# Optimization experiments

Hardware: AMD Instinct MI355X
Metric: run time of the kernel (lower is better)

## Reference

```python
import jax, jax.numpy as jnp
import numpy as np

B, T, C, Hh, Ww = 4, 24, 128, 48, 48
N_HEAD, D_K, D_MODEL = 16, 4, 128
D_PE = D_MODEL // N_HEAD  # 8
T_PERIOD = 1000.0


def group_norm(x, gamma, beta, groups, eps=1e-5):
    # x: (N, C) or (N, C, L); normalize over each group's channels (+ trailing dims)
    shp = x.shape
    xg = x.reshape(shp[0], groups, -1)
    mu = xg.mean(-1, keepdims=True)
    var = xg.var(-1, keepdims=True)
    xn = ((xg - mu) * jax.lax.rsqrt(var + eps)).reshape(shp)
    bshape = (1, shp[1]) + (1,) * (len(shp) - 2)
    return xn * gamma.reshape(bshape) + beta.reshape(bshape)


def _lin(k, fi, fo, std):
    kw, _ = jax.random.split(k)
    return jax.random.normal(kw, (fo, fi), jnp.float32) * std, jnp.zeros((fo,), jnp.float32)


def setup_inputs():
    key = jax.random.key(0)
    ks = jax.random.split(key, 8)
    std_k = float(np.sqrt(2.0 / D_K))
    p = {}
    p['x'] = jax.random.normal(ks[0], (B, T, C, Hh, Ww), jnp.float32)
    p['batch_positions'] = jnp.sort(jax.random.randint(ks[1], (B, T), 0, 365), axis=1).astype(jnp.int32)
    # inconv: 128 -> 256 -> 128, each Linear + GroupNorm(4) + ReLU
    p['w_in0'], p['b_in0'] = _lin(ks[2], C, 256, float(np.sqrt(2.0 / C)))
    p['g_in0'], p['be_in0'] = jnp.ones((256,), jnp.float32), jnp.zeros((256,), jnp.float32)
    p['w_in1'], p['b_in1'] = _lin(ks[3], 256, D_MODEL, float(np.sqrt(2.0 / 256)))
    p['g_in1'], p['be_in1'] = jnp.ones((D_MODEL,), jnp.float32), jnp.zeros((D_MODEL,), jnp.float32)
    # in_norm GroupNorm(16, 128)
    p['g_innorm'], p['b_innorm'] = jnp.ones((D_MODEL,), jnp.float32), jnp.zeros((D_MODEL,), jnp.float32)
    # attention: fixed query + key projection
    p['Q'] = jax.random.normal(ks[4], (N_HEAD, D_K), jnp.float32) * std_k
    p['w_k'], p['b_k'] = _lin(ks[5], D_MODEL, N_HEAD * D_K, std_k)
    # output MLP: 128 -> 256 -> 128
    p['w_m0'], p['b_m0'] = _lin(ks[6], D_MODEL, 256, float(np.sqrt(2.0 / D_MODEL)))
    p['g_m0'], p['be_m0'] = jnp.ones((256,), jnp.float32), jnp.zeros((256,), jnp.float32)
    p['w_m1'], p['b_m1'] = _lin(ks[7], 256, 128, float(np.sqrt(2.0 / 256)))
    p['g_m1'], p['be_m1'] = jnp.ones((128,), jnp.float32), jnp.zeros((128,), jnp.float32)
    # out_norm GroupNorm(16, 128)
    p['g_out'], p['b_out'] = jnp.ones((128,), jnp.float32), jnp.zeros((128,), jnp.float32)
    return p


def ltae_forward(x, pos_f, w_in0, b_in0, g_in0, be_in0, w_in1, b_in1, g_in1, be_in1,
                 g_innorm, b_innorm, Q, w_k, b_k,
                 w_m0, b_m0, g_m0, be_m0, w_m1, b_m1, g_m1, be_m1, g_out, b_out):
    Bsz, Ts, Cc, Hp, Wp = x.shape
    N = Bsz * Hp * Wp
    # (B,T,C,H,W) -> (B,H,W,T,C) -> (N, T, C): one sequence per pixel
    out = x.transpose(0, 3, 4, 1, 2).reshape(N, Ts, Cc)
    # inconv MLP on flattened tokens
    h = out.reshape(N * Ts, Cc)
    h = jax.nn.relu(group_norm(h @ w_in0.T + b_in0, g_in0, be_in0, 4))
    h = jax.nn.relu(group_norm(h @ w_in1.T + b_in1, g_in1, be_in1, 4))
    out = h.reshape(N, Ts, D_MODEL)
    # in_norm: GroupNorm(n_head) over (C, T)
    out = group_norm(out.transpose(0, 2, 1), g_innorm, b_innorm, N_HEAD).transpose(0, 2, 1)
    # positional encoding (d_model//n_head sinusoid, tiled n_head times)
    idx = jnp.arange(D_PE)
    denom = T_PERIOD ** (2.0 * (idx // 2).astype(jnp.float32) / D_PE)
    tab = pos_f[:, :, None] / denom  # (B, T, D_PE)
    tab = jnp.where(idx % 2 == 0, jnp.sin(tab), jnp.cos(tab))
    pe = jnp.tile(tab, (1, 1, N_HEAD))  # (B, T, D_MODEL)
    out = (out.reshape(Bsz, Hp * Wp, Ts, D_MODEL) + pe[:, None]).reshape(N, Ts, D_MODEL)
    # fixed-query multi-head attention
    k = (out @ w_k.T + b_k).reshape(N, Ts, N_HEAD, D_K)
    scores = jnp.einsum('hk,nthk->nht', Q, k) / jnp.sqrt(jnp.float32(D_K))
    a = jax.nn.softmax(scores, axis=-1)  # (N, H, T)
    v = out.reshape(N, Ts, N_HEAD, D_MODEL // N_HEAD)
    o = jnp.einsum('nht,nthv->nhv', a, v).reshape(N, D_MODEL)
    # output MLP + out_norm
    m = jax.nn.relu(group_norm(o @ w_m0.T + b_m0, g_m0, be_m0, 4))
    m = jax.nn.relu(group_norm(m @ w_m1.T + b_m1, g_m1, be_m1, 4))
    y = group_norm(m, g_out, b_out, N_HEAD)
    return y.reshape(Bsz, Hp, Wp, -1).transpose(0, 3, 1, 2)  # (B, C_out, H, W)


def reference(x, batch_positions, w_in0, b_in0, g_in0, be_in0, w_in1, b_in1, g_in1, be_in1,
              g_innorm, b_innorm, Q, w_k, b_k,
              w_m0, b_m0, g_m0, be_m0, w_m1, b_m1, g_m1, be_m1, g_out, b_out):
    pos_f = batch_positions.astype(jnp.float32)
    return ltae_forward(x, pos_f, w_in0, b_in0, g_in0, be_in0, w_in1, b_in1, g_in1, be_in1,
                        g_innorm, b_innorm, Q, w_k, b_k,
                        w_m0, b_m0, g_m0, be_m0, w_m1, b_m1, g_m1, be_m1, g_out, b_out)
```

## Files before the change

kernel.cpp:

```cpp
#include <hip/hip_runtime.h>
#include <math.h>

typedef _Float16 f16x8 __attribute__((ext_vector_type(8)));
typedef float f32x4 __attribute__((ext_vector_type(4)));
typedef unsigned short ushort_t;

constexpr int HWp = 2304;
constexpr float EPS = 1e-5f;

constexpr size_t M0P_OFF = 273472;
constexpr size_t M1P_OFF = 404544;
constexpr size_t OWS_OFF = 535616;

__device__ __forceinline__ int sidx(int row, int c) {
    return ((row << 8) + ((c << 1) ^ ((row & 7) << 4))) >> 1;
}
__device__ __forceinline__ int sidx2(int row, int c) {
    return ((row << 7) + ((c << 1) ^ ((row & 7) << 4))) >> 1;
}

__global__ void ltae_prep(const float* __restrict__ w_in0, const float* __restrict__ w_in1,
                          const float* __restrict__ Qm, const float* __restrict__ w_k,
                          const float* __restrict__ b_k, const int* __restrict__ bpos,
                          const float* __restrict__ w_m0, const float* __restrict__ w_m1,
                          _Float16* __restrict__ w1h, _Float16* __restrict__ w1l,
                          _Float16* __restrict__ w2h, _Float16* __restrict__ w2l,
                          _Float16* __restrict__ qkBh, _Float16* __restrict__ qkBl,
                          float* __restrict__ qb2G, float* __restrict__ peG,
                          float* __restrict__ w_m0P, float* __restrict__ w_m1P) {
    int i = blockIdx.x * 256 + threadIdx.x;
    if (i < 32768) {
        float v = w_in0[i];
        _Float16 h = (_Float16)v;
        w1h[i] = h; w1l[i] = (_Float16)(v - (float)h);
    } else if (i < 65536) {
        int j = i - 32768;
        float v = w_in1[j];
        _Float16 h = (_Float16)v;
        w2h[j] = h; w2l[j] = (_Float16)(v - (float)h);
    } else if (i < 67584) {
        int j = i - 65536; int h = j >> 7, k = j & 127;
        float s = 0.f;
        #pragma unroll
        for (int dk = 0; dk < 4; dk++) s = fmaf(Qm[h * 4 + dk], w_k[(h * 4 + dk) * 128 + k], s);
        s *= 0.5f;
        _Float16 hi = (_Float16)s;
        int ks = k >> 5, lg = (k >> 3) & 3, jj = k & 7;
        int pos = ((ks * 4 + lg) * 16 + h) * 8 + jj;
        qkBh[pos] = hi; qkBl[pos] = (_Float16)(s - (float)hi);
    } else if (i < 67600) {
        int h = i - 67584;
        float s = 0.f;
        #pragma unroll
        for (int dk = 0; dk < 4; dk++) s = fmaf(Qm[h * 4 + dk], b_k[h * 4 + dk], s);
        qb2G[h] = 0.5f * s;
    } else if (i < 68368) {
        int j = i - 67600;
        int bb = j / 192, r = j - bb * 192;
        int t = r >> 3, d = r & 7;
        const float dens[4] = {1.0f, 5.623413251903491f, 31.622776601683793f, 177.82794100389228f};
        float ang = (float)bpos[bb * 24 + t] / dens[d >> 1];
        peG[j] = (d & 1) ? cosf(ang) : sinf(ang);
    } else if (i < 101136) {
        int j = i - 68368;
        int c2 = j >> 9, rem = j & 511, o = rem >> 1, jj = rem & 1;
        w_m0P[j] = w_m0[o * 128 + c2 * 2 + jj];
    } else if (i < 133904) {
        int j = i - 101136;
        int c2 = j >> 8, rem = j & 255, o = rem >> 1, jj = rem & 1;
        w_m1P[j] = w_m1[o * 256 + c2 * 2 + jj];
    }
}

__global__ __launch_bounds__(256, 3) void ltae_main(
    const float* __restrict__ x,
    const float* __restrict__ b_in0, const float* __restrict__ g_in0, const float* __restrict__ be_in0,
    const float* __restrict__ b_in1, const float* __restrict__ g_in1, const float* __restrict__ be_in1,
    const float* __restrict__ g_innorm, const float* __restrict__ b_innorm,
    const _Float16* __restrict__ w1h, const _Float16* __restrict__ w1l,
    const _Float16* __restrict__ w2h, const _Float16* __restrict__ w2l,
    const _Float16* __restrict__ qkBh, const _Float16* __restrict__ qkBl,
    const float* __restrict__ qb2G, const float* __restrict__ peG,
    float* __restrict__ o_ws)
{
    __shared__ __align__(16) ushort_t Ah[48 * 128], Al[48 * 128];
    __shared__ __align__(16) ushort_t Hh[48 * 64], Hl[48 * 64];
    __shared__ float peS[24][8];
    __shared__ float2 partS[192];

    float* scP = (float*)Hh;

    const int tid = threadIdx.x;
    const int bid = blockIdx.x;
    const int sb  = (bid & 7) * 576 + (bid >> 3);
    const int b   = sb / 1152;
    const int pixbase = (sb - b * 1152) * 2;
    const int w  = tid >> 6;
    const int l  = tid & 63;
    const int lr = l & 15;
    const int lg = l >> 4;

    if (tid < 192) peS[tid >> 3][tid & 7] = peG[b * 192 + tid];
    for (int i = tid; i < 24 * 128; i += 256) {
        int t = i >> 7, c = i & 127;
        const float* gp = x + ((size_t)((b * 24 + t) * 128 + c)) * HWp + pixbase;
        float2 v = *(const float2*)gp;
        _Float16 h0 = (_Float16)v.x;
        _Float16 h1 = (_Float16)v.y;
        int i0 = sidx(t, c), i1 = sidx(24 + t, c);
        Ah[i0] = __builtin_bit_cast(ushort_t, h0);
        Al[i0] = __builtin_bit_cast(ushort_t, (_Float16)(v.x - (float)h0));
        Ah[i1] = __builtin_bit_cast(ushort_t, h1);
        Al[i1] = __builtin_bit_cast(ushort_t, (_Float16)(v.y - (float)h1));
    }
    __syncthreads();

    f32x4 acc2[3][2];
    #pragma unroll
    for (int m = 0; m < 3; m++)
        #pragma unroll
        for (int nt = 0; nt < 2; nt++) acc2[m][nt] = f32x4{0.f, 0.f, 0.f, 0.f};
    const int n2 = w * 32 + lr;

    #pragma unroll 1
    for (int q = 0; q < 4; q++) {
        const int n1 = q * 64 + w * 16 + lr;
        f16x8 bh[4], bl[4];
        #pragma unroll
        for (int ks = 0; ks < 4; ks++) {
            bh[ks] = *(const f16x8*)(w1h + n1 * 128 + ks * 32 + lg * 8);
            bl[ks] = *(const f16x8*)(w1l + n1 * 128 + ks * 32 + lg * 8);
        }
        const float gg = g_in0[n1], bb = be_in0[n1], bi = b_in0[n1];

        f32x4 acc1[3];
        #pragma unroll
        for (int m = 0; m < 3; m++) acc1[m] = f32x4{0.f, 0.f, 0.f, 0.f};
        #pragma unroll
        for (int m = 0; m < 3; m++) {
            #pragma unroll
            for (int ks = 0; ks < 4; ks++) {
                f16x8 ah = *(const f16x8*)&Ah[sidx(m * 16 + lr, ks * 32 + lg * 8)];
                f16x8 al = *(const f16x8*)&Al[sidx(m * 16 + lr, ks * 32 + lg * 8)];
                acc1[m] = __builtin_amdgcn_mfma_f32_16x16x32_f16(ah, bl[ks], acc1[m], 0, 0, 0);
                acc1[m] = __builtin_amdgcn_mfma_f32_16x16x32_f16(al, bh[ks], acc1[m], 0, 0, 0);
                acc1[m] = __builtin_amdgcn_mfma_f32_16x16x32_f16(ah, bh[ks], acc1[m], 0, 0, 0);
            }
        }
        float ps[3][4], ps2[3][4];
        #pragma unroll
        for (int m = 0; m < 3; m++) {
            #pragma unroll
            for (int r = 0; r < 4; r++) {
                float v = acc1[m][r] + bi;
                float s = v, s2 = v * v;
                #pragma unroll
                for (int mk = 1; mk <= 8; mk <<= 1) { s += __shfl_xor(s, mk); s2 += __shfl_xor(s2, mk); }
                ps[m][r] = s; ps2[m][r] = s2;
            }
        }
        if (lr == 0) {
            #pragma unroll
            for (int m = 0; m < 3; m++)
                #pragma unroll
                for (int r = 0; r < 4; r++)
                    partS[w * 48 + m * 16 + lg * 4 + r] = make_float2(ps[m][r], ps2[m][r]);
        }
        __syncthreads();
        #pragma unroll
        for (int m = 0; m < 3; m++) {
            #pragma unroll
            for (int r = 0; r < 4; r++) {
                int idx = m * 16 + lg * 4 + r;
                float st = 0.f, s2t = 0.f;
                #pragma unroll
                for (int j = 0; j < 4; j++) {
                    float2 qv = partS[j * 48 + idx];
                    st += qv.x; s2t += qv.y;
                }
                float mu = st * (1.f / 64.f);
                float rs = rsqrtf(s2t * (1.f / 64.f) - mu * mu + EPS);
                float v = acc1[m][r] + bi;
                float hv = fmaxf(fmaf((v - mu) * rs, gg, bb), 0.f);
                _Float16 h16 = (_Float16)hv;
                int ii = sidx2(idx, w * 16 + lr);
                Hh[ii] = __builtin_bit_cast(ushort_t, h16);
                Hl[ii] = __builtin_bit_cast(ushort_t, (_Float16)(hv - (float)h16));
            }
        }
        __syncthreads();

        f16x8 b2h[2][2], b2l[2][2];
        #pragma unroll
        for (int nt = 0; nt < 2; nt++) {
            int n = n2 + nt * 16;
            #pragma unroll
            for (int ks = 0; ks < 2; ks++) {
                b2h[nt][ks] = *(const f16x8*)(w2h + n * 256 + q * 64 + ks * 32 + lg * 8);
                b2l[nt][ks] = *(const f16x8*)(w2l + n * 256 + q * 64 + ks * 32 + lg * 8);
            }
        }
        #pragma unroll
        for (int m = 0; m < 3; m++) {
            #pragma unroll
            for (int ks = 0; ks < 2; ks++) {
                f16x8 ah = *(const f16x8*)&Hh[sidx2(m * 16 + lr, ks * 32 + lg * 8)];
                f16x8 al = *(const f16x8*)&Hl[sidx2(m * 16 + lr, ks * 32 + lg * 8)];
                #pragma unroll
                for (int nt = 0; nt < 2; nt++) {
                    acc2[m][nt] = __builtin_amdgcn_mfma_f32_16x16x32_f16(ah, b2l[nt][ks], acc2[m][nt], 0, 0, 0);
                    acc2[m][nt] = __builtin_amdgcn_mfma_f32_16x16x32_f16(al, b2h[nt][ks], acc2[m][nt], 0, 0, 0);
                    acc2[m][nt] = __builtin_amdgcn_mfma_f32_16x16x32_f16(ah, b2h[nt][ks], acc2[m][nt], 0, 0, 0);
                }
            }
        }
        __syncthreads();
    }

    {
        const int cA = w * 32 + lr;
        const int cB = cA + 16;
        float b2v[2]  = {b_in1[cA], b_in1[cB]};
        float g2v[2]  = {g_in1[cA], g_in1[cB]};
        float be2v[2] = {be_in1[cA], be_in1[cB]};
        float giV[2]  = {g_innorm[cA], g_innorm[cB]};
        float biV[2]  = {b_innorm[cA], b_innorm[cB]};

        float hv[3][4][2];
        #pragma unroll
        for (int m = 0; m < 3; m++) {
            #pragma unroll
            for (int r = 0; r < 4; r++) {
                float v0 = acc2[m][0][r] + b2v[0], v1 = acc2[m][1][r] + b2v[1];
                float s = v0 + v1, s2 = v0 * v0 + v1 * v1;
                #pragma unroll
                for (int mk = 1; mk <= 8; mk <<= 1) { s += __shfl_xor(s, mk); s2 += __shfl_xor(s2, mk); }
                float mu = s * (1.f / 32.f);
                float rs = rsqrtf(s2 * (1.f / 32.f) - mu * mu + EPS);
                hv[m][r][0] = fmaxf(fmaf((v0 - mu) * rs, g2v[0], be2v[0]), 0.f);
                hv[m][r][1] = fmaxf(fmaf((v1 - mu) * rs, g2v[1], be2v[1]), 0.f);
            }
        }
        float s0[2] = {0.f, 0.f}, s02[2] = {0.f, 0.f};
        float s1[2] = {0.f, 0.f}, s12[2] = {0.f, 0.f};
        #pragma unroll
        for (int m = 0; m < 3; m++) {
            #pragma unroll
            for (int r = 0; r < 4; r++) {
                int row = m * 16 + lg * 4 + r;
                #pragma unroll
                for (int nt = 0; nt < 2; nt++) {
                    float v = hv[m][r][nt];
                    if (row >= 24) { s1[nt] += v; s12[nt] += v * v; }
                    else           { s0[nt] += v; s02[nt] += v * v; }
                }
            }
        }
        #pragma unroll
        for (int nt = 0; nt < 2; nt++) {
            #pragma unroll
            for (int mk = 0; mk < 5; mk++) {
                int msk = (mk < 3) ? (1 << mk) : (2 << mk);
                s0[nt] += __shfl_xor(s0[nt], msk);  s02[nt] += __shfl_xor(s02[nt], msk);
                s1[nt] += __shfl_xor(s1[nt], msk);  s12[nt] += __shfl_xor(s12[nt], msk);
            }
        }
        float mu0[2], rs0[2], mu1[2], rs1[2];
        #pragma unroll
        for (int nt = 0; nt < 2; nt++) {
            mu0[nt] = s0[nt] * (1.f / 192.f);
            rs0[nt] = rsqrtf(s02[nt] * (1.f / 192.f) - mu0[nt] * mu0[nt] + EPS);
            mu1[nt] = s1[nt] * (1.f / 192.f);
            rs1[nt] = rsqrtf(s12[nt] * (1.f / 192.f) - mu1[nt] * mu1[nt] + EPS);
        }
        #pragma unroll
        for (int m = 0; m < 3; m++) {
            #pragma unroll
            for (int r = 0; r < 4; r++) {
                int row = m * 16 + lg * 4 + r;
                int p1 = row >= 24;
                int t = row - (p1 ? 24 : 0);
                float pe = peS[t][lr & 7];
                #pragma unroll
                for (int nt = 0; nt < 2; nt++) {
                    float mu = p1 ? mu1[nt] : mu0[nt];
                    float rs = p1 ? rs1[nt] : rs0[nt];
                    float v = fmaf((hv[m][r][nt] - mu) * rs, giV[nt], biV[nt]) + pe;
                    _Float16 h16 = (_Float16)v;
                    int ii = sidx(row, w * 32 + nt * 16 + lr);
                    Ah[ii] = __builtin_bit_cast(ushort_t, h16);
                    Al[ii] = __builtin_bit_cast(ushort_t, (_Float16)(v - (float)h16));
                }
            }
        }
    }
    __syncthreads();

    if (w < 3) {
        const int m = w;
        f16x8 qh[4], ql[4];
        #pragma unroll
        for (int ks = 0; ks < 4; ks++) {
            qh[ks] = *(const f16x8*)(qkBh + ((ks * 4 + lg) * 16 + lr) * 8);
            ql[ks] = *(const f16x8*)(qkBl + ((ks * 4 + lg) * 16 + lr) * 8);
        }
        f32x4 sacc = f32x4{0.f, 0.f, 0.f, 0.f};
        #pragma unroll
        for (int ks = 0; ks < 4; ks++) {
            f16x8 ah = *(const f16x8*)&Ah[sidx(m * 16 + lr, ks * 32 + lg * 8)];
            f16x8 al = *(const f16x8*)&Al[sidx(m * 16 + lr, ks * 32 + lg * 8)];
            sacc = __builtin_amdgcn_mfma_f32_16x16x32_f16(ah, ql[ks], sacc, 0, 0, 0);
            sacc = __builtin_amdgcn_mfma_f32_16x16x32_f16(al, qh[ks], sacc, 0, 0, 0);
            sacc = __builtin_amdgcn_mfma_f32_16x16x32_f16(ah, qh[ks], sacc, 0, 0, 0);
        }
        float qb = qb2G[lr];
        #pragma unroll
        for (int r = 0; r < 4; r++) {
            int row = m * 16 + lg * 4 + r;
            int p = row >= 24 ? 1 : 0;
            int t = row - p * 24;
            scP[(p * 16 + lr) * 24 + t] = sacc[r] + qb;
        }
    }
    __syncthreads();

    {
        const int p = w >> 1;
        int h = (w & 1) * 8 + (l >> 3), j = l & 7;
        float* sp = scP + (p * 16 + h) * 24;
        float mx = -1e30f;
        #pragma unroll
        for (int k = 0; k < 3; k++) mx = fmaxf(mx, sp[j + 8 * k]);
        mx = fmaxf(mx, __shfl_xor(mx, 1));
        mx = fmaxf(mx, __shfl_xor(mx, 2));
        mx = fmaxf(mx, __shfl_xor(mx, 4));
        float ev[3], sum = 0.f;
        #pragma unroll
        for (int k = 0; k < 3; k++) { ev[k] = __expf(sp[j + 8 * k] - mx); sum += ev[k]; }
        sum += __shfl_xor(sum, 1);
        sum += __shfl_xor(sum, 2);
        sum += __shfl_xor(sum, 4);
        float inv = 1.f / sum;
        #pragma unroll
        for (int k = 0; k < 3; k++) sp[j + 8 * k] = ev[k] * inv;
    }

    {
        const int p = w >> 1;
        int ch = (w & 1) * 64 + l;
        int h = ch >> 3;
        const float* sp = scP + (p * 16 + h) * 24;
        float s = 0.f;
        #pragma unroll
        for (int t = 0; t < 24; t++) {
            int ii = sidx(p * 24 + t, ch);
            float v = (float)__builtin_bit_cast(_Float16, Ah[ii]) +
                      (float)__builtin_bit_cast(_Float16, Al[ii]);
            s = fmaf(sp[t], v, s);
        }
        o_ws[((size_t)(b * 2304 + pixbase + p)) * 128 + ch] = s;
    }
}

__global__ __launch_bounds__(256) void ltae_mlp(
    const float* __restrict__ o_ws,
    const float* __restrict__ w_m0P, const float* __restrict__ b_m0,
    const float* __restrict__ g_m0, const float* __restrict__ be_m0,
    const float* __restrict__ w_m1P, const float* __restrict__ b_m1,
    const float* __restrict__ g_m1, const float* __restrict__ be_m1,
    const float* __restrict__ g_out, const float* __restrict__ b_out,
    float* __restrict__ out)
{
    __shared__ float ovP[8 * 128];
    __shared__ float mmP[8 * 256];
    float* ysP = ovP;

    const int tid = threadIdx.x;
    const int bid = blockIdx.x;
    const int b = bid / 288;
    const int pix8 = (bid - b * 288) * 8;

    #pragma unroll
    for (int k = 0; k < 4; k++) {
        int i = tid + (k << 8);
        ovP[i] = o_ws[((size_t)(b * 2304 + pix8)) * 128 + i];
    }
    __syncthreads();

    {
        const int o = tid;
        float acc[8];
        #pragma unroll
        for (int pp = 0; pp < 8; pp++) acc[pp] = 0.f;
        for (int c2 = 0; c2 < 64; c2++) {
            float2 w2 = *(const float2*)(w_m0P + c2 * 512 + o * 2);
            #pragma unroll
            for (int pp = 0; pp < 8; pp++) {
                float2 x2 = *(const float2*)(ovP + pp * 128 + c2 * 2);
                acc[pp] = fmaf(w2.x, x2.x, acc[pp]);
                acc[pp] = fmaf(w2.y, x2.y, acc[pp]);
            }
        }
        float bi = b_m0[o], gg = g_m0[o], bb = be_m0[o];
        #pragma unroll
        for (int pp = 0; pp < 8; pp++) {
            float v = acc[pp] + bi;
            float s = v, s2 = v * v;
            #pragma unroll
            for (int mk = 1; mk <= 32; mk <<= 1) { s += __shfl_xor(s, mk); s2 += __shfl_xor(s2, mk); }
            float mu = s * (1.f / 64.f);
            float rs = rsqrtf(s2 * (1.f / 64.f) - mu * mu + EPS);
            mmP[pp * 256 + o] = fmaxf(fmaf((v - mu) * rs, gg, bb), 0.f);
        }
    }
    __syncthreads();

    {
        const int o = tid & 127, hw = tid >> 7;
        float acc[4];
        #pragma unroll
        for (int q = 0; q < 4; q++) acc[q] = 0.f;
        for (int c2 = 0; c2 < 128; c2++) {
            float2 w2 = *(const float2*)(w_m1P + c2 * 256 + o * 2);
            #pragma unroll
            for (int q = 0; q < 4; q++) {
                float2 x2 = *(const float2*)(mmP + (hw * 4 + q) * 256 + c2 * 2);
                acc[q] = fmaf(w2.x, x2.x, acc[q]);
                acc[q] = fmaf(w2.y, x2.y, acc[q]);
            }
        }
        float bm1 = b_m1[o], gm1 = g_m1[o], bem1 = be_m1[o];
        float go = g_out[o], bo = b_out[o];
        #pragma unroll
        for (int q = 0; q < 4; q++) {
            const int pp = hw * 4 + q;
            float v = acc[q] + bm1;
            float s = v, s2 = v * v;
            #pragma unroll
            for (int mk = 1; mk <= 16; mk <<= 1) { s += __shfl_xor(s, mk); s2 += __shfl_xor(s2, mk); }
            float mu = s * (1.f / 32.f);
            float rs = rsqrtf(s2 * (1.f / 32.f) - mu * mu + EPS);
            float v2 = fmaxf(fmaf((v - mu) * rs, gm1, bem1), 0.f);
            float t1 = v2, t2 = v2 * v2;
            #pragma unroll
            for (int mk = 1; mk <= 4; mk <<= 1) { t1 += __shfl_xor(t1, mk); t2 += __shfl_xor(t2, mk); }
            float mu2 = t1 * (1.f / 8.f);
            float rs2 = rsqrtf(t2 * (1.f / 8.f) - mu2 * mu2 + EPS);
            ysP[pp * 128 + o] = fmaf((v2 - mu2) * rs2, go, bo);
        }
    }
    __syncthreads();

    {
        const int o = tid & 127, q4 = (tid >> 7) * 4;
        float4 y4;
        y4.x = ysP[(q4 + 0) * 128 + o];
        y4.y = ysP[(q4 + 1) * 128 + o];
        y4.z = ysP[(q4 + 2) * 128 + o];
        y4.w = ysP[(q4 + 3) * 128 + o];
        *(float4*)(out + ((size_t)(b * 128 + o)) * HWp + pix8 + q4) = y4;
    }
}

extern "C" void kernel_launch(void* const* d_in, const int* in_sizes, int n_in,
                              void* d_out, int out_size, void* d_ws, size_t ws_size,
                              hipStream_t stream) {
    const float* x        = (const float*)d_in[0];
    const int*   bpos     = (const int*)  d_in[1];
    const float* w_in0    = (const float*)d_in[2];
    const float* b_in0    = (const float*)d_in[3];
    const float* g_in0    = (const float*)d_in[4];
    const float* be_in0   = (const float*)d_in[5];
    const float* w_in1    = (const float*)d_in[6];
    const float* b_in1    = (const float*)d_in[7];
    const float* g_in1    = (const float*)d_in[8];
    const float* be_in1   = (const float*)d_in[9];
    const float* g_innorm = (const float*)d_in[10];
    const float* b_innorm = (const float*)d_in[11];
    const float* Qm       = (const float*)d_in[12];
    const float* w_k      = (const float*)d_in[13];
    const float* b_k      = (const float*)d_in[14];
    const float* w_m0     = (const float*)d_in[15];
    const float* b_m0     = (const float*)d_in[16];
    const float* g_m0     = (const float*)d_in[17];
    const float* be_m0    = (const float*)d_in[18];
    const float* w_m1     = (const float*)d_in[19];
    const float* b_m1     = (const float*)d_in[20];
    const float* g_m1     = (const float*)d_in[21];
    const float* be_m1    = (const float*)d_in[22];
    const float* g_out    = (const float*)d_in[23];
    const float* b_out    = (const float*)d_in[24];

    _Float16* w1h   = (_Float16*)d_ws;
    _Float16* w1l   = w1h + 32768;
    _Float16* w2h   = w1l + 32768;
    _Float16* w2l   = w2h + 32768;
    _Float16* qkBh  = (_Float16*)((char*)d_ws + 262144);
    _Float16* qkBl  = qkBh + 2048;
    float*    qb2G  = (float*)((char*)d_ws + 270336);
    float*    peG   = (float*)((char*)d_ws + 270400);
    float*    w_m0P = (float*)((char*)d_ws + M0P_OFF);
    float*    w_m1P = (float*)((char*)d_ws + M1P_OFF);
    float*    o_ws  = (float*)((char*)d_ws + OWS_OFF);

    hipLaunchKernelGGL(ltae_prep, dim3(524), dim3(256), 0, stream,
                       w_in0, w_in1, Qm, w_k, b_k, bpos, w_m0, w_m1,
                       w1h, w1l, w2h, w2l, qkBh, qkBl, qb2G, peG, w_m0P, w_m1P);

    hipLaunchKernelGGL(ltae_main, dim3(4608), dim3(256), 0, stream,
                       x,
                       b_in0, g_in0, be_in0,
                       b_in1, g_in1, be_in1,
                       g_innorm, b_innorm,
                       w1h, w1l, w2h, w2l, qkBh, qkBl, qb2G, peG,
                       o_ws);

    hipLaunchKernelGGL(ltae_mlp, dim3(1152), dim3(256), 0, stream,
                       o_ws,
                       w_m0P, b_m0, g_m0, be_m0,
                       w_m1P, b_m1, g_m1, be_m1,
                       g_out, b_out,
                       (float*)d_out);
}
```

Before: 309.4 us.

## Repartition first inconv GEMM by rows per wave to drop cross-wave GroupNorm reduction

```diff
diff --git a/kernel.cpp b/kernel.cpp
--- a/kernel.cpp
+++ b/kernel.cpp
@@ -86,7 +86,6 @@
     __shared__ __align__(16) ushort_t Ah[48 * 128], Al[48 * 128];
     __shared__ __align__(16) ushort_t Hh[48 * 64], Hl[48 * 64];
     __shared__ float peS[24][8];
-    __shared__ float2 partS[192];
 
     float* scP = (float*)Hh;
 
@@ -121,71 +120,59 @@
         #pragma unroll
         for (int nt = 0; nt < 2; nt++) acc2[m][nt] = f32x4{0.f, 0.f, 0.f, 0.f};
     const int n2 = w * 32 + lr;
+    const int arow = w * 12 + (lr < 12 ? lr : 0);
 
     #pragma unroll 1
     for (int q = 0; q < 4; q++) {
-        const int n1 = q * 64 + w * 16 + lr;
-        f16x8 bh[4], bl[4];
+        f16x8 ahh[4], alw[4];
         #pragma unroll
         for (int ks = 0; ks < 4; ks++) {
-            bh[ks] = *(const f16x8*)(w1h + n1 * 128 + ks * 32 + lg * 8);
-            bl[ks] = *(const f16x8*)(w1l + n1 * 128 + ks * 32 + lg * 8);
-        }
-        const float gg = g_in0[n1], bb = be_in0[n1], bi = b_in0[n1];
-
-        f32x4 acc1[3];
-        #pragma unroll
-        for (int m = 0; m < 3; m++) acc1[m] = f32x4{0.f, 0.f, 0.f, 0.f};
-        #pragma unroll
-        for (int m = 0; m < 3; m++) {
+            ahh[ks] = *(const f16x8*)&Ah[sidx(arow, ks * 32 + lg * 8)];
+            alw[ks] = *(const f16x8*)&Al[sidx(arow, ks * 32 + lg * 8)];
+        }
+        f32x4 acc1[4];
+        float bi[4], gg[4], bb[4];
+        #pragma unroll
+        for (int nt = 0; nt < 4; nt++) {
+            const int n1 = q * 64 + nt * 16 + lr;
+            f16x8 bh[4], bl[4];
             #pragma unroll
             for (int ks = 0; ks < 4; ks++) {
-                f16x8 ah = *(const f16x8*)&Ah[sidx(m * 16 + lr, ks * 32 + lg * 8)];
-                f16x8 al = *(const f16x8*)&Al[sidx(m * 16 + lr, ks * 32 + lg * 8)];
-                acc1[m] = __builtin_amdgcn_mfma_f32_16x16x32_f16(ah, bl[ks], acc1[m], 0, 0, 0);
-                acc1[m] = __builtin_amdgcn_mfma_f32_16x16x32_f16(al, bh[ks], acc1[m], 0, 0, 0);
-                acc1[m] = __builtin_amdgcn_mfma_f32_16x16x32_f16(ah, bh[ks], acc1[m], 0, 0, 0);
-            }
-        }
-        float ps[3][4], ps2[3][4];
-        #pragma unroll
-        for (int m = 0; m < 3; m++) {
-            #pragma unroll
-            for (int r = 0; r < 4; r++) {
-                float v = acc1[m][r] + bi;
-                float s = v, s2 = v * v;
+                bh[ks] = *(const f16x8*)(w1h + n1 * 128 + ks * 32 + lg * 8);
+                bl[ks] = *(const f16x8*)(w1l + n1 * 128 + ks * 32 + lg * 8);
+            }
+            bi[nt] = b_in0[n1]; gg[nt] = g_in0[n1]; bb[nt] = be_in0[n1];
+            f32x4 a = f32x4{0.f, 0.f, 0.f, 0.f};
+            #pragma unroll
+            for (int ks = 0; ks < 4; ks++) {
+                a = __builtin_amdgcn_mfma_f32_16x16x32_f16(ahh[ks], bl[ks], a, 0, 0, 0);
+                a = __builtin_amdgcn_mfma_f32_16x16x32_f16(alw[ks], bh[ks], a, 0, 0, 0);
+                a = __builtin_amdgcn_mfma_f32_16x16x32_f16(ahh[ks], bh[ks], a, 0, 0, 0);
+            }
+            acc1[nt] = a;
+        }
+        #pragma unroll
+        for (int r = 0; r < 4; r++) {
+            float v0 = acc1[0][r] + bi[0], v1 = acc1[1][r] + bi[1];
+            float v2 = acc1[2][r] + bi[2], v3 = acc1[3][r] + bi[3];
+            float s = v0 + v1 + v2 + v3;
+            float s2 = v0 * v0 + v1 * v1 + v2 * v2 + v3 * v3;
+            #pragma unroll
+            for (int mk = 1; mk <= 8; mk <<= 1) { s += __shfl_xor(s, mk); s2 += __shfl_xor(s2, mk); }
+            float mu = s * (1.f / 64.f);
+            float rs = rsqrtf(s2 * (1.f / 64.f) - mu * mu + EPS);
+            int tloc = lg * 4 + r;
+            if (tloc < 12) {
+                int row = w * 12 + tloc;
+                float vv[4] = {v0, v1, v2, v3};
                 #pragma unroll
-                for (int mk = 1; mk <= 8; mk <<= 1) { s += __shfl_xor(s, mk); s2 += __shfl_xor(s2, mk); }
-                ps[m][r] = s; ps2[m][r] = s2;
-            }
-        }
-        if (lr == 0) {
-            #pragma unroll
-            for (int m = 0; m < 3; m++)
-                #pragma unroll
-                for (int r = 0; r < 4; r++)
-                    partS[w * 48 + m * 16 + lg * 4 + r] = make_float2(ps[m][r], ps2[m][r]);
-        }
-        __syncthreads();
-        #pragma unroll
-        for (int m = 0; m < 3; m++) {
-            #pragma unroll
-            for (int r = 0; r < 4; r++) {
-                int idx = m * 16 + lg * 4 + r;
-                float st = 0.f, s2t = 0.f;
-                #pragma unroll
-                for (int j = 0; j < 4; j++) {
-                    float2 qv = partS[j * 48 + idx];
-                    st += qv.x; s2t += qv.y;
+                for (int nt = 0; nt < 4; nt++) {
+                    float hv = fmaxf(fmaf((vv[nt] - mu) * rs, gg[nt], bb[nt]), 0.f);
+                    _Float16 h16 = (_Float16)hv;
+                    int ii = sidx2(row, nt * 16 + lr);
+                    Hh[ii] = __builtin_bit_cast(ushort_t, h16);
+                    Hl[ii] = __builtin_bit_cast(ushort_t, (_Float16)(hv - (float)h16));
                 }
-                float mu = st * (1.f / 64.f);
-                float rs = rsqrtf(s2t * (1.f / 64.f) - mu * mu + EPS);
-                float v = acc1[m][r] + bi;
-                float hv = fmaxf(fmaf((v - mu) * rs, gg, bb), 0.f);
-                _Float16 h16 = (_Float16)hv;
-                int ii = sidx2(idx, w * 16 + lr);
-                Hh[ii] = __builtin_bit_cast(ushort_t, h16);
-                Hl[ii] = __builtin_bit_cast(ushort_t, (_Float16)(hv - (float)h16));
             }
         }
         __syncthreads();
```

Result: slower. 439.9 us (+42.2%).
